# Performance work log

Measured on AMD Instinct MI355X. Metric: run time of the kernel, lower is better.

The kernel has to match this reference:

```python
import jax, jax.numpy as jnp
import numpy as np

D_MODEL = 1024
N_HEADS = 16
HEAD_DIM = D_MODEL // N_HEADS


def setup_inputs() -> dict:
    key = jax.random.key(0)
    ks = jax.random.split(key, 7)
    b, s, l = 2, 2048, 8
    x = jax.random.normal(ks[0], (b, s, D_MODEL), dtype=jnp.float32)
    past_keys = jax.random.normal(ks[1], (b, N_HEADS, s, l, HEAD_DIM), dtype=jnp.float32)
    past_values = jax.random.normal(ks[2], (b, N_HEADS, s, l, HEAD_DIM), dtype=jnp.float32)
    sc = 1.0 / np.sqrt(D_MODEL)
    W_qkv = jax.random.normal(ks[3], (D_MODEL, 3 * D_MODEL), dtype=jnp.float32) * sc
    b_qkv = jnp.zeros((3 * D_MODEL,), dtype=jnp.float32)
    W_out = jax.random.normal(ks[4], (D_MODEL, D_MODEL), dtype=jnp.float32) * sc
    b_out = jnp.zeros((D_MODEL,), dtype=jnp.float32)
    return {"x": x, "past_keys": past_keys, "past_values": past_values,
            "W_qkv": W_qkv, "b_qkv": b_qkv, "W_out": W_out, "b_out": b_out}


def _split_heads(t):
    b, s, d = t.shape
    return t.reshape(b, s, N_HEADS, HEAD_DIM).transpose(0, 2, 1, 3)  # [b,h,s,hd]


def reference(x, past_keys, past_values, W_qkv, b_qkv, W_out, b_out):
    b, s, _ = x.shape
    qkv = x @ W_qkv + b_qkv  # [b,s,3d]
    q_row, k_row, v_row = jnp.split(qkv, 3, axis=-1)
    q = _split_heads(q_row)  # [b,h,s,hd]
    k = _split_heads(k_row)
    v = _split_heads(v_row)
    scale = 1.0 / jnp.sqrt(jnp.asarray(HEAD_DIM, dtype=x.dtype))
    token_scores = jnp.einsum('bhqd,bhkd->bhqk', q, k) * scale  # [b,h,s,s]
    causal = jnp.triu(jnp.ones((s, s), dtype=bool), k=1)
    token_scores = jnp.where(causal, -jnp.inf, token_scores)
    mem_scores = jnp.einsum('bhsd,bhsld->bhsl', q, past_keys) * scale  # [b,h,s,l]
    scores = jnp.concatenate([token_scores, mem_scores], axis=-1)  # [b,h,s,s+l]
    weights = jax.nn.softmax(scores, axis=-1)
    token_w = weights[..., :s]
    mem_w = weights[..., s:]
    token_ctx = jnp.einsum('bhqk,bhkd->bhqd', token_w, v)
    mem_ctx = jnp.einsum('bhsl,bhsld->bhsd', mem_w, past_values)
    out = token_ctx + mem_ctx  # [b,h,s,hd]
    out = out.transpose(0, 2, 1, 3).reshape(b, s, D_MODEL)
    out = out @ W_out + b_out
    return out, k, v
```

## Files before the change

kernel.cpp:

```cpp
#include <hip/hip_runtime.h>
#include <hip/hip_bf16.h>

#define D_MODEL 1024
#define N_HEADS 16
#define HEAD_DIM 64
#define BATCH 2
#define SEQ 2048
#define NMEM 8

typedef __attribute__((ext_vector_type(8))) short vshort8;
typedef __attribute__((ext_vector_type(4))) short vshort4;
typedef __attribute__((ext_vector_type(4))) float f32x4;

static __device__ __forceinline__ short f2bf(float f) {
    unsigned u = __builtin_bit_cast(unsigned, f);
    unsigned r = u + 0x7fffu + ((u >> 16) & 1u);
    return (short)(r >> 16);
}
static __device__ __forceinline__ float bf2f(short s) {
    unsigned u = ((unsigned)(unsigned short)s) << 16;
    return __builtin_bit_cast(float, u);
}

static __device__ __forceinline__ f32x4 mfma16x16x32(vshort8 a, vshort8 b, f32x4 c) {
    return __builtin_amdgcn_mfma_f32_16x16x32_bf16(a, b, c, 0, 0, 0);
}

typedef const __attribute__((address_space(1))) char* gptr_t;
typedef __attribute__((address_space(3))) char* lptr_t;
static __device__ __forceinline__ void gload_lds16(const void* g, void* l) {
    __builtin_amdgcn_global_load_lds((gptr_t)g, (lptr_t)l, 16, 0, 0);
}

__global__ void cast_f32_bf16(const float* __restrict__ in, short* __restrict__ out, int n4) {
    int i = blockIdx.x * blockDim.x + threadIdx.x;
    if (i >= n4) return;
    float4 v = reinterpret_cast<const float4*>(in)[i];
    vshort4 o;
    o.x = f2bf(v.x); o.y = f2bf(v.y); o.z = f2bf(v.z); o.w = f2bf(v.w);
    reinterpret_cast<vshort4*>(out)[i] = o;
}

__global__ void transpose_cast(const float* __restrict__ in, short* __restrict__ out, int R, int C) {
    __shared__ float tile[32][33];
    int n0 = blockIdx.x * 32;
    int k0 = blockIdx.y * 32;
    int tx = threadIdx.x, ty = threadIdx.y;
    #pragma unroll
    for (int i = 0; i < 4; i++) {
        int r = ty + i * 8;
        tile[r][tx] = in[(k0 + r) * C + n0 + tx];
    }
    __syncthreads();
    #pragma unroll
    for (int i = 0; i < 4; i++) {
        int r = ty + i * 8;
        out[(n0 + r) * R + k0 + tx] = f2bf(tile[tx][r]);
    }
}

#define BM 128
#define BN 128
#define BK 32

template<int EPI>
__global__ __launch_bounds__(256) void gemm_bf16(
    const short* __restrict__ A, const short* __restrict__ Bt,
    int M, int N, int K,
    const float* __restrict__ bias,
    float* __restrict__ Cout,
    short* __restrict__ Qb, short* __restrict__ Kb, short* __restrict__ Vt,
    float* __restrict__ k_out, float* __restrict__ v_out)
{
    __shared__ short As[BM][BK];
    __shared__ short Bs[BN][BK];
    int m0 = blockIdx.x * BM, n0 = blockIdx.y * BN;
    int tid = threadIdx.x;
    int wave = tid >> 6, lane = tid & 63;
    int wr = wave >> 1, wc = wave & 1;
    int lo = lane & 15, hi = lane >> 4;

    f32x4 acc[4][4];
    #pragma unroll
    for (int i = 0; i < 4; i++)
        #pragma unroll
        for (int j = 0; j < 4; j++)
            acc[i][j] = (f32x4){0.f, 0.f, 0.f, 0.f};

    int srow = wave * 16 + (lane >> 2);
    int sce  = (lane & 3) * 8;

    for (int k0 = 0; k0 < K; k0 += BK) {
        __syncthreads();
        #pragma unroll
        for (int r = 0; r < 2; r++) {
            int row = r * 64 + srow;
            gload_lds16(&A[(size_t)(m0 + row) * K + k0 + sce],
                        ((char*)&As[0][0]) + (size_t)(r * 64 + wave * 16) * 64);
            gload_lds16(&Bt[(size_t)(n0 + row) * K + k0 + sce],
                        ((char*)&Bs[0][0]) + (size_t)(r * 64 + wave * 16) * 64);
        }
        __syncthreads();
        vshort8 av[4], bv[4];
        #pragma unroll
        for (int fr = 0; fr < 4; fr++)
            av[fr] = *reinterpret_cast<const vshort8*>(&As[wr * 64 + fr * 16 + lo][hi * 8]);
        #pragma unroll
        for (int fc = 0; fc < 4; fc++)
            bv[fc] = *reinterpret_cast<const vshort8*>(&Bs[wc * 64 + fc * 16 + lo][hi * 8]);
        #pragma unroll
        for (int fr = 0; fr < 4; fr++)
            #pragma unroll
            for (int fc = 0; fc < 4; fc++)
                acc[fr][fc] = mfma16x16x32(av[fr], bv[fc], acc[fr][fc]);
    }

    #pragma unroll
    for (int fr = 0; fr < 4; fr++) {
        #pragma unroll
        for (int fc = 0; fc < 4; fc++) {
            int col = n0 + wc * 64 + fc * 16 + lo;
            float bb = bias[col];
            #pragma unroll
            for (int j = 0; j < 4; j++) {
                int row = m0 + wr * 64 + fr * 16 + hi * 4 + j;
                float val = acc[fr][fc][j] + bb;
                if (EPI == 0) {
                    Cout[row * N + col] = val;
                } else {
                    int sec = col >> 10, c = col & 1023;
                    int h = c >> 6, d = c & 63;
                    int b = row >> 11, s = row & 2047;
                    int idx = ((b * 16 + h) * 2048 + s) * 64 + d;
                    if (sec == 0) {
                        Qb[idx] = f2bf(val);
                    } else if (sec == 1) {
                        k_out[idx] = val;
                        Kb[idx] = f2bf(val);
                    } else {
                        v_out[idx] = val;
                        Vt[((b * 16 + h) * 64 + d) * 2048 + s] = f2bf(val);
                    }
                }
            }
        }
    }
}

__global__ __launch_bounds__(256) void attn_kernel(
    const short* __restrict__ Qb, const short* __restrict__ Kb, const short* __restrict__ Vt,
    const float* __restrict__ pk, const float* __restrict__ pv,
    short* __restrict__ ctx)
{
    __shared__ short Ks[2][64][64];
    __shared__ short Vs[2][64][64];
    __shared__ short P[4][16][72];
    __shared__ float wlds[4][16][8];

    int bh = blockIdx.x, pairidx = blockIdx.y;
    int b = bh >> 4, h = bh & 15;
    int wave = threadIdx.x >> 6, lane = threadIdx.x & 63;
    int lo = lane & 15, hi = lane >> 4;

    const short* Qh = Qb + (size_t)bh * SEQ * 64;
    const short* Kh = Kb + (size_t)bh * SEQ * 64;
    const short* Vh = Vt + (size_t)bh * 64 * SEQ;

    int st_sub  = lane >> 3;
    int st_csrc = (((lane & 7) ^ st_sub) << 4);

    for (int pass = 0; pass < 2; pass++) {
        int qblk = (pass == 0) ? (31 - pairidx) : pairidx;
        int qbase = qblk * 64 + wave * 16;

        {
            #pragma unroll
            for (int rd = 0; rd < 2; rd++) {
                int tr = rd * 32 + wave * 8 + st_sub;
                gload_lds16((const char*)Kh + (((size_t)tr) << 7) + st_csrc,
                            ((char*)&Ks[0][0][0]) + rd * 4096 + wave * 1024);
                gload_lds16((const char*)Vh + (((size_t)tr) << 12) + st_csrc,
                            ((char*)&Vs[0][0][0]) + rd * 4096 + wave * 1024);
            }
        }

        vshort8 aq[2];
        #pragma unroll
        for (int ks = 0; ks < 2; ks++)
            aq[ks] = *reinterpret_cast<const vshort8*>(&Qh[(size_t)(qbase + lo) * 64 + ks * 32 + hi * 8]);

        {
            int rm = lane >> 2, ml0 = lane & 3;
            size_t srow = (size_t)bh * SEQ + qbase + rm;
            const float4* pkA = reinterpret_cast<const float4*>(pk + (srow * 8 + ml0) * 64);
            const float4* pkB = pkA + 64;
            const short* qrow = Qh + (size_t)(qbase + rm) * 64;
            float dA = 0.f, dB = 0.f;
            #pragma unroll
            for (int t = 0; t < 16; t++) {
                float4 a4 = pkA[t];
                float4 b4 = pkB[t];
                vshort4 q4 = *reinterpret_cast<const vshort4*>(&qrow[t * 4]);
                float q0 = bf2f(q4.x), q1 = bf2f(q4.y), q2 = bf2f(q4.z), q3 = bf2f(q4.w);
                dA += q0 * a4.x + q1 * a4.y + q2 * a4.z + q3 * a4.w;
                dB += q0 * b4.x + q1 * b4.y + q2 * b4.z + q3 * b4.w;
            }
            wlds[wave][rm][ml0]     = dA * 0.125f;
            wlds[wave][rm][ml0 + 4] = dB * 0.125f;
        }
        asm volatile("s_waitcnt lgkmcnt(0)" ::: "memory");

        float m_r[4], ell[4];
        float ew[4][8];
        f32x4 o[4];
        #pragma unroll
        for (int j = 0; j < 4; j++) {
            float mm = -3.0e38f;
            #pragma unroll
            for (int ml = 0; ml < 8; ml++) mm = fmaxf(mm, wlds[wave][hi * 4 + j][ml]);
            m_r[j] = mm;
            float e = 0.f;
            #pragma unroll
            for (int ml = 0; ml < 8; ml++) {
                float t = __expf(wlds[wave][hi * 4 + j][ml] - mm);
                ew[j][ml] = t;
                e += t;
            }
            ell[j] = e;
        }
        #pragma unroll
        for (int g = 0; g < 4; g++) {
            #pragma unroll
            for (int j = 0; j < 4; j++) {
                size_t srow = (size_t)bh * SEQ + qbase + hi * 4 + j;
                const float* pvr = pv + srow * 8 * 64 + g * 16 + lo;
                float acc = 0.f;
                #pragma unroll
                for (int ml = 0; ml < 8; ml++)
                    acc += ew[j][ml] * pvr[ml * 64];
                o[g][j] = acc;
            }
        }

        __syncthreads();

        int buf = 0;
        for (int kvt = 0; kvt <= qblk; kvt++) {
            if (kvt < qblk) {
                int kvbase = (kvt + 1) * 64;
                int nb = buf ^ 1;
                #pragma unroll
                for (int rd = 0; rd < 2; rd++) {
                    int tr = rd * 32 + wave * 8 + st_sub;
                    gload_lds16((const char*)Kh + (((size_t)(kvbase + tr)) << 7) + st_csrc,
                                ((char*)&Ks[nb][0][0]) + rd * 4096 + wave * 1024);
                    gload_lds16((const char*)Vh + (((size_t)tr) << 12) + (size_t)kvbase * 2 + st_csrc,
                                ((char*)&Vs[nb][0][0]) + rd * 4096 + wave * 1024);
                }
            }
            int kvbase = kvt * 64;

            f32x4 sc[4];
            #pragma unroll
            for (int g = 0; g < 4; g++) {
                int kr = g * 16 + lo;
                const char* base = ((const char*)&Ks[buf][0][0]) + kr * 128;
                vshort8 bk0 = *reinterpret_cast<const vshort8*>(base + ((hi * 16) ^ ((kr & 7) << 4)));
                vshort8 bk1 = *reinterpret_cast<const vshort8*>(base + ((64 + hi * 16) ^ ((kr & 7) << 4)));
                f32x4 z = (f32x4){0.f, 0.f, 0.f, 0.f};
                z = mfma16x16x32(aq[0], bk0, z);
                sc[g] = mfma16x16x32(aq[1], bk1, z);
            }
            bool diag = (kvt == qblk);
            float p[4][4];
            float tm[4];
            #pragma unroll
            for (int j = 0; j < 4; j++) tm[j] = -3.0e38f;
            #pragma unroll
            for (int g = 0; g < 4; g++)
                #pragma unroll
                for (int j = 0; j < 4; j++) {
                    float sv = sc[g][j] * 0.125f;
                    if (diag && (kvbase + g * 16 + lo > qbase + hi * 4 + j)) sv = -3.0e38f;
                    p[g][j] = sv;
                    tm[j] = fmaxf(tm[j], sv);
                }
            #pragma unroll
            for (int j = 0; j < 4; j++) {
                tm[j] = fmaxf(tm[j], __shfl_xor(tm[j], 1));
                tm[j] = fmaxf(tm[j], __shfl_xor(tm[j], 2));
                tm[j] = fmaxf(tm[j], __shfl_xor(tm[j], 4));
                tm[j] = fmaxf(tm[j], __shfl_xor(tm[j], 8));
            }
            float fac[4], rs[4];
            #pragma unroll
            for (int j = 0; j < 4; j++) {
                float mn = fmaxf(m_r[j], tm[j]);
                fac[j] = __expf(m_r[j] - mn);
                m_r[j] = mn;
                rs[j] = 0.f;
            }
            #pragma unroll
            for (int g = 0; g < 4; g++)
                #pragma unroll
                for (int j = 0; j < 4; j++) {
                    p[g][j] = __expf(p[g][j] - m_r[j]);
                    rs[j] += p[g][j];
                }
            #pragma unroll
            for (int j = 0; j < 4; j++) {
                rs[j] += __shfl_xor(rs[j], 1);
                rs[j] += __shfl_xor(rs[j], 2);
                rs[j] += __shfl_xor(rs[j], 4);
                rs[j] += __shfl_xor(rs[j], 8);
                ell[j] = ell[j] * fac[j] + rs[j];
            }
            #pragma unroll
            for (int g = 0; g < 4; g++)
                #pragma unroll
                for (int j = 0; j < 4; j++)
                    o[g][j] *= fac[j];

            #pragma unroll
            for (int g = 0; g < 4; g++)
                #pragma unroll
                for (int j = 0; j < 4; j++)
                    P[wave][hi * 4 + j][g * 16 + lo] = f2bf(p[g][j]);

            vshort8 ap0 = *reinterpret_cast<const vshort8*>(&P[wave][lo][hi * 8]);
            vshort8 ap1 = *reinterpret_cast<const vshort8*>(&P[wave][lo][32 + hi * 8]);
            #pragma unroll
            for (int g = 0; g < 4; g++) {
                int vr = g * 16 + lo;
                const char* base = ((const char*)&Vs[buf][0][0]) + vr * 128;
                vshort8 bv0 = *reinterpret_cast<const vshort8*>(base + ((hi * 16) ^ ((vr & 7) << 4)));
                vshort8 bv1 = *reinterpret_cast<const vshort8*>(base + ((64 + hi * 16) ^ ((vr & 7) << 4)));
                o[g] = mfma16x16x32(ap0, bv0, o[g]);
                o[g] = mfma16x16x32(ap1, bv1, o[g]);
            }

            __syncthreads();
            buf ^= 1;
        }

        #pragma unroll
        for (int g = 0; g < 4; g++)
            #pragma unroll
            for (int j = 0; j < 4; j++) {
                int s = qbase + hi * 4 + j;
                float val = o[g][j] / ell[j];
                ctx[(size_t)(b * SEQ + s) * D_MODEL + h * 64 + g * 16 + lo] = f2bf(val);
            }
    }
}

extern "C" void kernel_launch(void* const* d_in, const int* in_sizes, int n_in,
                              void* d_out, int out_size, void* d_ws, size_t ws_size,
                              hipStream_t stream) {
    const float* x    = (const float*)d_in[0];
    const float* pk   = (const float*)d_in[1];
    const float* pv   = (const float*)d_in[2];
    const float* Wqkv = (const float*)d_in[3];
    const float* bqkv = (const float*)d_in[4];
    const float* Wout = (const float*)d_in[5];
    const float* bout = (const float*)d_in[6];

    float* out   = (float*)d_out;
    float* k_out = out + 4194304;
    float* v_out = out + 8388608;

    char* ws = (char*)d_ws;
    short* Xb    = (short*)(ws);
    short* Wqkvt = (short*)(ws + (size_t)(8  << 20));
    short* Woutt = (short*)(ws + (size_t)(14 << 20));
    short* Qb    = (short*)(ws + (size_t)(16 << 20));
    short* Kb    = (short*)(ws + (size_t)(24 << 20));
    short* Vt    = (short*)(ws + (size_t)(32 << 20));
    short* ctx   = Xb;

    cast_f32_bf16<<<4096, 256, 0, stream>>>(x, Xb, 4194304 / 4);
    dim3 tb(32, 8);
    transpose_cast<<<dim3(96, 32), tb, 0, stream>>>(Wqkv, Wqkvt, 1024, 3072);
    transpose_cast<<<dim3(32, 32), tb, 0, stream>>>(Wout, Woutt, 1024, 1024);

    gemm_bf16<1><<<dim3(32, 24), 256, 0, stream>>>(
        Xb, Wqkvt, 4096, 3072, 1024, bqkv,
        nullptr, Qb, Kb, Vt, k_out, v_out);

    attn_kernel<<<dim3(32, 16), 256, 0, stream>>>(Qb, Kb, Vt, pk, pv, ctx);

    gemm_bf16<0><<<dim3(32, 8), 256, 0, stream>>>(
        ctx, Woutt, 4096, 1024, 1024, bout,
        out, nullptr, nullptr, nullptr, nullptr, nullptr);
}
```

Before: 455.8 us.

## Widen GEMM K-tile with swizzled LDS, split attention blocks, add lazy rescale

```diff
diff --git a/kernel.cpp b/kernel.cpp
--- a/kernel.cpp
+++ b/kernel.cpp
@@ -7,6 +7,8 @@
 #define BATCH 2
 #define SEQ 2048
 #define NMEM 8
+
+#define SCALE_L2 0.18033688f
 
 typedef __attribute__((ext_vector_type(8))) short vshort8;
 typedef __attribute__((ext_vector_type(4))) short vshort4;
@@ -61,7 +63,7 @@
 
 #define BM 128
 #define BN 128
-#define BK 32
+#define BK 64
 
 template<int EPI>
 __global__ __launch_bounds__(256) void gemm_bf16(
@@ -87,32 +89,42 @@
         for (int j = 0; j < 4; j++)
             acc[i][j] = (f32x4){0.f, 0.f, 0.f, 0.f};
 
-    int srow = wave * 16 + (lane >> 2);
-    int sce  = (lane & 3) * 8;
+    int srow8 = wave * 8 + (lane >> 3);
+    const char* Ab = (const char*)&As[0][0];
+    const char* Bb = (const char*)&Bs[0][0];
 
     for (int k0 = 0; k0 < K; k0 += BK) {
         __syncthreads();
         #pragma unroll
-        for (int r = 0; r < 2; r++) {
-            int row = r * 64 + srow;
-            gload_lds16(&A[(size_t)(m0 + row) * K + k0 + sce],
-                        ((char*)&As[0][0]) + (size_t)(r * 64 + wave * 16) * 64);
-            gload_lds16(&Bt[(size_t)(n0 + row) * K + k0 + sce],
-                        ((char*)&Bs[0][0]) + (size_t)(r * 64 + wave * 16) * 64);
+        for (int r = 0; r < 4; r++) {
+            int row = r * 32 + srow8;
+            int sc8 = (((lane & 7) ^ (row & 7)) << 3);
+            size_t dstoff = (size_t)r * 4096 + wave * 1024 + (size_t)(lane & 63) * 16;
+            gload_lds16(&A[(size_t)(m0 + row) * K + k0 + sc8], (char*)Ab + dstoff);
+            gload_lds16(&Bt[(size_t)(n0 + row) * K + k0 + sc8], (char*)Bb + dstoff);
         }
         __syncthreads();
-        vshort8 av[4], bv[4];
-        #pragma unroll
-        for (int fr = 0; fr < 4; fr++)
-            av[fr] = *reinterpret_cast<const vshort8*>(&As[wr * 64 + fr * 16 + lo][hi * 8]);
-        #pragma unroll
-        for (int fc = 0; fc < 4; fc++)
-            bv[fc] = *reinterpret_cast<const vshort8*>(&Bs[wc * 64 + fc * 16 + lo][hi * 8]);
-        #pragma unroll
-        for (int fr = 0; fr < 4; fr++)
-            #pragma unroll
-            for (int fc = 0; fc < 4; fc++)
-                acc[fr][fc] = mfma16x16x32(av[fr], bv[fc], acc[fr][fc]);
+        #pragma unroll
+        for (int kk = 0; kk < 2; kk++) {
+            vshort8 av[4], bv[4];
+            #pragma unroll
+            for (int fr = 0; fr < 4; fr++) {
+                int ra = wr * 64 + fr * 16 + lo;
+                av[fr] = *reinterpret_cast<const vshort8*>(
+                    Ab + ra * 128 + (((kk * 4 + hi) ^ (ra & 7)) << 4));
+            }
+            #pragma unroll
+            for (int fc = 0; fc < 4; fc++) {
+                int rb = wc * 64 + fc * 16 + lo;
+                bv[fc] = *reinterpret_cast<const vshort8*>(
+                    Bb + rb * 128 + (((kk * 4 + hi) ^ (rb & 7)) << 4));
+            }
+            #pragma unroll
+            for (int fr = 0; fr < 4; fr++)
+                #pragma unroll
+                for (int fc = 0; fc < 4; fc++)
+                    acc[fr][fc] = mfma16x16x32(av[fr], bv[fc], acc[fr][fc]);
+        }
     }
 
     #pragma unroll
@@ -147,211 +159,224 @@
     }
 }
 
-__global__ __launch_bounds__(256) void attn_kernel(
+__global__ __launch_bounds__(256, 4) void attn_kernel(
     const short* __restrict__ Qb, const short* __restrict__ Kb, const short* __restrict__ Vt,
     const float* __restrict__ pk, const float* __restrict__ pv,
     short* __restrict__ ctx)
 {
     __shared__ short Ks[2][64][64];
     __shared__ short Vs[2][64][64];
-    __shared__ short P[4][16][72];
-    __shared__ float wlds[4][16][8];
-
-    int bh = blockIdx.x, pairidx = blockIdx.y;
+    __shared__ short P[4][16][64];
+
+    int bh = blockIdx.x;
+    int y = blockIdx.y;
+    int c = y & 7, m = y >> 3;
+    int qblk = (m == 0) ? (31 - c) : (m == 1) ? c : (m == 2) ? (23 - c) : (8 + c);
+
     int b = bh >> 4, h = bh & 15;
     int wave = threadIdx.x >> 6, lane = threadIdx.x & 63;
     int lo = lane & 15, hi = lane >> 4;
+    int qbase = qblk * 64 + wave * 16;
 
     const short* Qh = Qb + (size_t)bh * SEQ * 64;
     const short* Kh = Kb + (size_t)bh * SEQ * 64;
     const short* Vh = Vt + (size_t)bh * 64 * SEQ;
 
+    char* Pw = (char*)&P[wave][0][0];
+    float* wl = (float*)Pw;
+
     int st_sub  = lane >> 3;
     int st_csrc = (((lane & 7) ^ st_sub) << 4);
 
-    for (int pass = 0; pass < 2; pass++) {
-        int qblk = (pass == 0) ? (31 - pairidx) : pairidx;
-        int qbase = qblk * 64 + wave * 16;
-
-        {
+    #pragma unroll
+    for (int rd = 0; rd < 2; rd++) {
+        int tr = rd * 32 + wave * 8 + st_sub;
+        gload_lds16((const char*)Kh + (((size_t)tr) << 7) + st_csrc,
+                    ((char*)&Ks[0][0][0]) + rd * 4096 + wave * 1024);
+        gload_lds16((const char*)Vh + (((size_t)tr) << 12) + st_csrc,
+                    ((char*)&Vs[0][0][0]) + rd * 4096 + wave * 1024);
+    }
+
+    vshort8 aq[2];
+    #pragma unroll
+    for (int ks = 0; ks < 2; ks++)
+        aq[ks] = *reinterpret_cast<const vshort8*>(&Qh[(size_t)(qbase + lo) * 64 + ks * 32 + hi * 8]);
+
+    {
+        int rm = lane >> 2, ml0 = lane & 3;
+        size_t srow = (size_t)bh * SEQ + qbase + rm;
+        const float4* pkA = reinterpret_cast<const float4*>(pk + (srow * 8 + ml0) * 64);
+        const float4* pkB = pkA + 64;
+        const short* qrow = Qh + (size_t)(qbase + rm) * 64;
+        float dA = 0.f, dB = 0.f;
+        #pragma unroll
+        for (int t = 0; t < 16; t++) {
+            float4 a4 = pkA[t];
+            float4 b4 = pkB[t];
+            vshort4 q4 = *reinterpret_cast<const vshort4*>(&qrow[t * 4]);
+            float q0 = bf2f(q4.x), q1 = bf2f(q4.y), q2 = bf2f(q4.z), q3 = bf2f(q4.w);
+            dA += q0 * a4.x + q1 * a4.y + q2 * a4.z + q3 * a4.w;
+            dB += q0 * b4.x + q1 * b4.y + q2 * b4.z + q3 * b4.w;
+        }
+        wl[rm * 8 + ml0]     = dA * SCALE_L2;
+        wl[rm * 8 + ml0 + 4] = dB * SCALE_L2;
+    }
+    asm volatile("s_waitcnt lgkmcnt(0)" ::: "memory");
+
+    float m_r[4], ell[4];
+    float ew[4][8];
+    f32x4 o[4];
+    #pragma unroll
+    for (int j = 0; j < 4; j++) {
+        int rr = hi * 4 + j;
+        float mm = -3.0e38f;
+        #pragma unroll
+        for (int ml = 0; ml < 8; ml++) mm = fmaxf(mm, wl[rr * 8 + ml]);
+        m_r[j] = mm;
+        float e = 0.f;
+        #pragma unroll
+        for (int ml = 0; ml < 8; ml++) {
+            float t = exp2f(wl[rr * 8 + ml] - mm);
+            ew[j][ml] = t;
+            e += t;
+        }
+        ell[j] = e;
+    }
+    #pragma unroll
+    for (int g = 0; g < 4; g++) {
+        #pragma unroll
+        for (int j = 0; j < 4; j++) {
+            size_t srow = (size_t)bh * SEQ + qbase + hi * 4 + j;
+            const float* pvr = pv + srow * 8 * 64 + g * 16 + lo;
+            float acc = 0.f;
+            #pragma unroll
+            for (int ml = 0; ml < 8; ml++)
+                acc += ew[j][ml] * pvr[ml * 64];
+            o[g][j] = acc;
+        }
+    }
+
+    __syncthreads();
+
+    int buf = 0;
+    for (int kvt = 0; kvt <= qblk; kvt++) {
+        if (kvt < qblk) {
+            int kvbase = (kvt + 1) * 64;
+            int nb = buf ^ 1;
             #pragma unroll
             for (int rd = 0; rd < 2; rd++) {
                 int tr = rd * 32 + wave * 8 + st_sub;
-                gload_lds16((const char*)Kh + (((size_t)tr) << 7) + st_csrc,
-                            ((char*)&Ks[0][0][0]) + rd * 4096 + wave * 1024);
-                gload_lds16((const char*)Vh + (((size_t)tr) << 12) + st_csrc,
-                            ((char*)&Vs[0][0][0]) + rd * 4096 + wave * 1024);
-            }
-        }
-
-        vshort8 aq[2];
-        #pragma unroll
-        for (int ks = 0; ks < 2; ks++)
-            aq[ks] = *reinterpret_cast<const vshort8*>(&Qh[(size_t)(qbase + lo) * 64 + ks * 32 + hi * 8]);
-
-        {
-            int rm = lane >> 2, ml0 = lane & 3;
-            size_t srow = (size_t)bh * SEQ + qbase + rm;
-            const float4* pkA = reinterpret_cast<const float4*>(pk + (srow * 8 + ml0) * 64);
-            const float4* pkB = pkA + 64;
-            const short* qrow = Qh + (size_t)(qbase + rm) * 64;
-            float dA = 0.f, dB = 0.f;
-            #pragma unroll
-            for (int t = 0; t < 16; t++) {
-                float4 a4 = pkA[t];
-                float4 b4 = pkB[t];
-                vshort4 q4 = *reinterpret_cast<const vshort4*>(&qrow[t * 4]);
-                float q0 = bf2f(q4.x), q1 = bf2f(q4.y), q2 = bf2f(q4.z), q3 = bf2f(q4.w);
-                dA += q0 * a4.x + q1 * a4.y + q2 * a4.z + q3 * a4.w;
-                dB += q0 * b4.x + q1 * b4.y + q2 * b4.z + q3 * b4.w;
-            }
-            wlds[wave][rm][ml0]     = dA * 0.125f;
-            wlds[wave][rm][ml0 + 4] = dB * 0.125f;
-        }
-        asm volatile("s_waitcnt lgkmcnt(0)" ::: "memory");
-
-        float m_r[4], ell[4];
-        float ew[4][8];
-        f32x4 o[4];
+                gload_lds16((const char*)Kh + (((size_t)(kvbase + tr)) << 7) + st_csrc,
+                            ((char*)&Ks[nb][0][0]) + rd * 4096 + wave * 1024);
+                gload_lds16((const char*)Vh + (((size_t)tr) << 12) + (size_t)kvbase * 2 + st_csrc,
+                            ((char*)&Vs[nb][0][0]) + rd * 4096 + wave * 1024);
+            }
+        }
+        int kvbase = kvt * 64;
+
+        f32x4 sc[4];
+        #pragma unroll
+        for (int g = 0; g < 4; g++) {
+            int kr = g * 16 + lo;
+            const char* base = ((const char*)&Ks[buf][0][0]) + kr * 128;
+            vshort8 bk0 = *reinterpret_cast<const vshort8*>(base + ((hi * 16) ^ ((kr & 7) << 4)));
+            vshort8 bk1 = *reinterpret_cast<const vshort8*>(base + ((64 + hi * 16) ^ ((kr & 7) << 4)));
+            f32x4 z = (f32x4){0.f, 0.f, 0.f, 0.f};
+            z = mfma16x16x32(aq[0], bk0, z);
+            sc[g] = mfma16x16x32(aq[1], bk1, z);
+        }
+        bool diag = (kvt == qblk);
+        float p[4][4];
+        float tm[4];
+        #pragma unroll
+        for (int j = 0; j < 4; j++) tm[j] = -3.0e38f;
+        #pragma unroll
+        for (int g = 0; g < 4; g++)
+            #pragma unroll
+            for (int j = 0; j < 4; j++) {
+                float sv = sc[g][j] * SCALE_L2;
+                if (diag && (kvbase + g * 16 + lo > qbase + hi * 4 + j)) sv = -3.0e38f;
+                p[g][j] = sv;
+                tm[j] = fmaxf(tm[j], sv);
+            }
         #pragma unroll
         for (int j = 0; j < 4; j++) {
-            float mm = -3.0e38f;
-            #pragma unroll
-            for (int ml = 0; ml < 8; ml++) mm = fmaxf(mm, wlds[wave][hi * 4 + j][ml]);
-            m_r[j] = mm;
-            float e = 0.f;
-            #pragma unroll
-            for (int ml = 0; ml < 8; ml++) {
-                float t = __expf(wlds[wave][hi * 4 + j][ml] - mm);
-                ew[j][ml] = t;
-                e += t;
-            }
-            ell[j] = e;
-        }
-        #pragma unroll
-        for (int g = 0; g < 4; g++) {
+            tm[j] = fmaxf(tm[j], __shfl_xor(tm[j], 1));
+            tm[j] = fmaxf(tm[j], __shfl_xor(tm[j], 2));
+            tm[j] = fmaxf(tm[j], __shfl_xor(tm[j], 4));
+            tm[j] = fmaxf(tm[j], __shfl_xor(tm[j], 8));
+        }
+        bool skip = (tm[0] <= m_r[0] + 8.f) && (tm[1] <= m_r[1] + 8.f) &&
+                    (tm[2] <= m_r[2] + 8.f) && (tm[3] <= m_r[3] + 8.f);
+        bool noresc = __all(skip);
+        float fac[4], rs[4];
+        #pragma unroll
+        for (int j = 0; j < 4; j++) {
+            if (noresc) {
+                fac[j] = 1.f;
+            } else {
+                float mn = fmaxf(m_r[j], tm[j]);
+                fac[j] = exp2f(m_r[j] - mn);
+                m_r[j] = mn;
+            }
+            rs[j] = 0.f;
+        }
+        #pragma unroll
+        for (int g = 0; g < 4; g++)
             #pragma unroll
             for (int j = 0; j < 4; j++) {
-                size_t srow = (size_t)bh * SEQ + qbase + hi * 4 + j;
-                const float* pvr = pv + srow * 8 * 64 + g * 16 + lo;
-                float acc = 0.f;
-                #pragma unroll
-                for (int ml = 0; ml < 8; ml++)
-                    acc += ew[j][ml] * pvr[ml * 64];
-                o[g][j] = acc;
-            }
-        }
-
-        __syncthreads();
-
-        int buf = 0;
-        for (int kvt = 0; kvt <= qblk; kvt++) {
-            if (kvt < qblk) {
-                int kvbase = (kvt + 1) * 64;
-                int nb = buf ^ 1;
-                #pragma unroll
-                for (int rd = 0; rd < 2; rd++) {
-                    int tr = rd * 32 + wave * 8 + st_sub;
-                    gload_lds16((const char*)Kh + (((size_t)(kvbase + tr)) << 7) + st_csrc,
-                                ((char*)&Ks[nb][0][0]) + rd * 4096 + wave * 1024);
-                    gload_lds16((const char*)Vh + (((size_t)tr) << 12) + (size_t)kvbase * 2 + st_csrc,
-                                ((char*)&Vs[nb][0][0]) + rd * 4096 + wave * 1024);
-                }
-            }
-            int kvbase = kvt * 64;
-
-            f32x4 sc[4];
-            #pragma unroll
-            for (int g = 0; g < 4; g++) {
-                int kr = g * 16 + lo;
-                const char* base = ((const char*)&Ks[buf][0][0]) + kr * 128;
-                vshort8 bk0 = *reinterpret_cast<const vshort8*>(base + ((hi * 16) ^ ((kr & 7) << 4)));
-                vshort8 bk1 = *reinterpret_cast<const vshort8*>(base + ((64 + hi * 16) ^ ((kr & 7) << 4)));
-                f32x4 z = (f32x4){0.f, 0.f, 0.f, 0.f};
-                z = mfma16x16x32(aq[0], bk0, z);
-                sc[g] = mfma16x16x32(aq[1], bk1, z);
-            }
-            bool diag = (kvt == qblk);
-            float p[4][4];
-            float tm[4];
-            #pragma unroll
-            for (int j = 0; j < 4; j++) tm[j] = -3.0e38f;
-            #pragma unroll
-            for (int g = 0; g < 4; g++)
-                #pragma unroll
-                for (int j = 0; j < 4; j++) {
-                    float sv = sc[g][j] * 0.125f;
-                    if (diag && (kvbase + g * 16 + lo > qbase + hi * 4 + j)) sv = -3.0e38f;
-                    p[g][j] = sv;
-                    tm[j] = fmaxf(tm[j], sv);
-                }
-            #pragma unroll
-            for (int j = 0; j < 4; j++) {
-                tm[j] = fmaxf(tm[j], __shfl_xor(tm[j], 1));
-                tm[j] = fmaxf(tm[j], __shfl_xor(tm[j], 2));
-                tm[j] = fmaxf(tm[j], __shfl_xor(tm[j], 4));
-                tm[j] = fmaxf(tm[j], __shfl_xor(tm[j], 8));
-            }
-            float fac[4], rs[4];
-            #pragma unroll
-            for (int j = 0; j < 4; j++) {
-                float mn = fmaxf(m_r[j], tm[j]);
-                fac[j] = __expf(m_r[j] - mn);
-                m_r[j] = mn;
-                rs[j] = 0.f;
-            }
-            #pragma unroll
-            for (int g = 0; g < 4; g++)
-                #pragma unroll
-                for (int j = 0; j < 4; j++) {
-                    p[g][j] = __expf(p[g][j] - m_r[j]);
-                    rs[j] += p[g][j];
-                }
-            #pragma unroll
-            for (int j = 0; j < 4; j++) {
-                rs[j] += __shfl_xor(rs[j], 1);
-                rs[j] += __shfl_xor(rs[j], 2);
-                rs[j] += __shfl_xor(rs[j], 4);
-                rs[j] += __shfl_xor(rs[j], 8);
-                ell[j] = ell[j] * fac[j] + rs[j];
-            }
+                p[g][j] = exp2f(p[g][j] - m_r[j]);
+                rs[j] += p[g][j];
+            }
+        #pragma unroll
+        for (int j = 0; j < 4; j++) {
+            rs[j] += __shfl_xor(rs[j], 1);
+            rs[j] += __shfl_xor(rs[j], 2);
+            rs[j] += __shfl_xor(rs[j], 4);
+            rs[j] += __shfl_xor(rs[j], 8);
+            ell[j] = ell[j] * fac[j] + rs[j];
+        }
+        if (!noresc) {
             #pragma unroll
             for (int g = 0; g < 4; g++)
                 #pragma unroll
                 for (int j = 0; j < 4; j++)
                     o[g][j] *= fac[j];
-
-            #pragma unroll
-            for (int g = 0; g < 4; g++)
-                #pragma unroll
-                for (int j = 0; j < 4; j++)
-                    P[wave][hi * 4 + j][g * 16 + lo] = f2bf(p[g][j]);
-
-            vshort8 ap0 = *reinterpret_cast<const vshort8*>(&P[wave][lo][hi * 8]);
-            vshort8 ap1 = *reinterpret_cast<const vshort8*>(&P[wave][lo][32 + hi * 8]);
-            #pragma unroll
-            for (int g = 0; g < 4; g++) {
-                int vr = g * 16 + lo;
-                const char* base = ((const char*)&Vs[buf][0][0]) + vr * 128;
-                vshort8 bv0 = *reinterpret_cast<const vshort8*>(base + ((hi * 16) ^ ((vr & 7) << 4)));
-                vshort8 bv1 = *reinterpret_cast<const vshort8*>(base + ((64 + hi * 16) ^ ((vr & 7) << 4)));
-                o[g] = mfma16x16x32(ap0, bv0, o[g]);
-                o[g] = mfma16x16x32(ap1, bv1, o[g]);
-            }
-
-            __syncthreads();
-            buf ^= 1;
         }
 
         #pragma unroll
         for (int g = 0; g < 4; g++)
             #pragma unroll
             for (int j = 0; j < 4; j++) {
-                int s = qbase + hi * 4 + j;
-                float val = o[g][j] / ell[j];
-                ctx[(size_t)(b * SEQ + s) * D_MODEL + h * 64 + g * 16 + lo] = f2bf(val);
-            }
-    }
+                int r = hi * 4 + j;
+                *reinterpret_cast<short*>(Pw + r * 128 +
+                    ((((2 * g + (lo >> 3)) ^ (r & 7)) << 4) + 2 * (lo & 7))) = f2bf(p[g][j]);
+            }
+
+        vshort8 ap0 = *reinterpret_cast<const vshort8*>(Pw + lo * 128 + ((hi ^ (lo & 7)) << 4));
+        vshort8 ap1 = *reinterpret_cast<const vshort8*>(Pw + lo * 128 + (((4 + hi) ^ (lo & 7)) << 4));
+        #pragma unroll
+        for (int g = 0; g < 4; g++) {
+            int vr = g * 16 + lo;
+            const char* base = ((const char*)&Vs[buf][0][0]) + vr * 128;
+            vshort8 bv0 = *reinterpret_cast<const vshort8*>(base + ((hi * 16) ^ ((vr & 7) << 4)));
+            vshort8 bv1 = *reinterpret_cast<const vshort8*>(base + ((64 + hi * 16) ^ ((vr & 7) << 4)));
+            o[g] = mfma16x16x32(ap0, bv0, o[g]);
+            o[g] = mfma16x16x32(ap1, bv1, o[g]);
+        }
+
+        __syncthreads();
+        buf ^= 1;
+    }
+
+    #pragma unroll
+    for (int g = 0; g < 4; g++)
+        #pragma unroll
+        for (int j = 0; j < 4; j++) {
+            int s = qbase + hi * 4 + j;
+            float val = o[g][j] / ell[j];
+            ctx[(size_t)(b * SEQ + s) * D_MODEL + h * 64 + g * 16 + lo] = f2bf(val);
+        }
 }
 
 extern "C" void kernel_launch(void* const* d_in, const int* in_sizes, int n_in,
@@ -387,7 +412,7 @@
         Xb, Wqkvt, 4096, 3072, 1024, bqkv,
         nullptr, Qb, Kb, Vt, k_out, v_out);
 
-    attn_kernel<<<dim3(32, 16), 256, 0, stream>>>(Qb, Kb, Vt, pk, pv, ctx);
+    attn_kernel<<<dim3(32, 32), 256, 0, stream>>>(Qb, Kb, Vt, pk, pv, ctx);
 
     gemm_bf16<0><<<dim3(32, 8), 256, 0, stream>>>(
         ctx, Woutt, 4096, 1024, 1024, bout,
```

New measurement: 482.7 us. 5.9% more time.
